# Optimization experiments

Hardware: AMD Instinct MI355X
Metric: run time of the kernel (lower is better)

The kernel has to match this reference:

```python
import jax, jax.numpy as jnp
from jax import lax
import numpy as np

B, C, H, W = 32, 256, 56, 56
R = max(1, C // 16)  # reduced channels = 16
K = 7                # spatial kernel


def setup_inputs() -> dict:
    key = jax.random.key(0)
    k_x, k1, k2, k3 = jax.random.split(key, 4)
    x = jax.random.normal(k_x, (B, C, H, W), dtype=jnp.float32)
    # shared MLP 1x1 convs (bias=False): stored as 2D matrices
    w1 = jax.random.normal(k1, (R, C), dtype=jnp.float32) * (1.0 / np.sqrt(C))
    w2 = jax.random.normal(k2, (C, R), dtype=jnp.float32) * (1.0 / np.sqrt(R))
    # spatial 7x7 conv: 2 in-channels (avg,max) -> 1 out, OIHW
    w_sp = jax.random.normal(k3, (1, 2, K, K), dtype=jnp.float32) * (1.0 / np.sqrt(2 * K * K))
    return {"x": x, "w1": w1, "w2": w2, "w_sp": w_sp}


def reference(x, w1, w2, w_sp):
    # ---- Channel attention ----
    avg = jnp.mean(x, axis=(2, 3))            # (B, C)
    mx = jnp.max(x, axis=(2, 3))              # (B, C)

    def mlp(v):  # shared 1x1-conv MLP on pooled vectors
        return jnp.einsum('cr,br->bc', w2, jax.nn.relu(jnp.einsum('rc,bc->br', w1, v)))

    ca = jax.nn.sigmoid(mlp(avg) + mlp(mx))[:, :, None, None]  # (B, C, 1, 1)
    xc = x * ca                                # (B, C, H, W)

    # ---- Spatial attention ----
    pooled = jnp.stack([jnp.mean(xc, axis=1), jnp.max(xc, axis=1)], axis=1)  # (B, 2, H, W)
    pad = (K - 1) // 2
    sa = jax.nn.sigmoid(
        lax.conv_general_dilated(pooled, w_sp, window_strides=(1, 1),
                                 padding=[(pad, pad), (pad, pad)],
                                 dimension_numbers=('NCHW', 'OIHW', 'NCHW')))  # (B, 1, H, W)

    # ---- Residual ----
    return x + xc * sa
```

## Files before the change

kernel.cpp:

```cpp
#include <hip/hip_runtime.h>
#include <math.h>

#define B_ 32
#define C_ 256
#define H_ 56
#define W_ 56
#define HW_ (H_*W_)
#define R_ 16
#define K_ 7

__device__ __forceinline__ float sigmoidf_(float v) { return 1.0f / (1.0f + expf(-v)); }

__global__ void k_pool_bc(const float* __restrict__ x,
                          float* __restrict__ avg, float* __restrict__ mx) {
    const int bc = blockIdx.x;
    const float4* xp = (const float4*)(x + (size_t)bc * HW_);
    float s = 0.0f, m = -INFINITY;
    for (int i = threadIdx.x; i < HW_ / 4; i += blockDim.x) {
        float4 v = xp[i];
        s += v.x + v.y + v.z + v.w;
        m = fmaxf(m, fmaxf(fmaxf(v.x, v.y), fmaxf(v.z, v.w)));
    }
    #pragma unroll
    for (int off = 32; off > 0; off >>= 1) {
        s += __shfl_down(s, off, 64);
        m  = fmaxf(m, __shfl_down(m, off, 64));
    }
    __shared__ float ss[4], sm[4];
    const int wave = threadIdx.x >> 6;
    if ((threadIdx.x & 63) == 0) { ss[wave] = s; sm[wave] = m; }
    __syncthreads();
    if (threadIdx.x == 0) {
        float S = ss[0] + ss[1] + ss[2] + ss[3];
        float M = fmaxf(fmaxf(sm[0], sm[1]), fmaxf(sm[2], sm[3]));
        avg[bc] = S * (1.0f / HW_);
        mx[bc]  = M;
    }
}

__global__ void k_mlp_ca(const float* __restrict__ avg, const float* __restrict__ mx,
                         const float* __restrict__ w1, const float* __restrict__ w2,
                         float* __restrict__ ca) {
    const int b = blockIdx.x;
    __shared__ float sa_[C_], sm_[C_], h_[R_];
    const int t = threadIdx.x;
    sa_[t] = avg[b * C_ + t];
    sm_[t] = mx[b * C_ + t];
    __syncthreads();
    if (t < R_) {
        float ha = 0.0f, hm = 0.0f;
        for (int c = 0; c < C_; ++c) {
            const float wv = w1[t * C_ + c];
            ha += wv * sa_[c];
            hm += wv * sm_[c];
        }
        h_[t] = fmaxf(ha, 0.0f) + fmaxf(hm, 0.0f);
    }
    __syncthreads();
    float acc = 0.0f;
    #pragma unroll
    for (int r = 0; r < R_; ++r) acc += w2[t * R_ + r] * h_[r];
    ca[b * C_ + t] = sigmoidf_(acc);
}

__global__ void k_spatial_pool(const float* __restrict__ x, const float* __restrict__ ca,
                               float* __restrict__ pooled) {
    const int idx = blockIdx.x * blockDim.x + threadIdx.x;
    if (idx >= B_ * (HW_ / 4)) return;
    const int b = idx / (HW_ / 4);
    const int q = idx % (HW_ / 4);
    const float4* xp = (const float4*)(x + (size_t)b * C_ * HW_);
    const float* cab = ca + b * C_;
    float4 s = {0.f, 0.f, 0.f, 0.f};
    float4 m = {-INFINITY, -INFINITY, -INFINITY, -INFINITY};
    for (int c = 0; c < C_; ++c) {
        const float a = cab[c];
        float4 v = xp[c * (HW_ / 4) + q];
        v.x *= a; v.y *= a; v.z *= a; v.w *= a;
        s.x += v.x; s.y += v.y; s.z += v.z; s.w += v.w;
        m.x = fmaxf(m.x, v.x); m.y = fmaxf(m.y, v.y);
        m.z = fmaxf(m.z, v.z); m.w = fmaxf(m.w, v.w);
    }
    const float inv = 1.0f / C_;
    float4 sm4 = {s.x * inv, s.y * inv, s.z * inv, s.w * inv};
    ((float4*)(pooled + (size_t)b * 2 * HW_))[q]      = sm4;
    ((float4*)(pooled + (size_t)b * 2 * HW_ + HW_))[q] = m;
}

__global__ void k_conv_sa(const float* __restrict__ pooled, const float* __restrict__ wsp,
                          float* __restrict__ sa) {
    __shared__ float wv[2 * K_ * K_];
    if (threadIdx.x < 2 * K_ * K_) wv[threadIdx.x] = wsp[threadIdx.x];
    __syncthreads();
    const int idx = blockIdx.x * blockDim.x + threadIdx.x;
    if (idx >= B_ * HW_) return;
    const int b = idx / HW_;
    const int hw = idx % HW_;
    const int h = hw / W_, w = hw % W_;
    const float* pa = pooled + (size_t)b * 2 * HW_;
    const float* pm = pa + HW_;
    float acc = 0.0f;
    #pragma unroll
    for (int ky = 0; ky < K_; ++ky) {
        const int y = h + ky - 3;
        if (y < 0 || y >= H_) continue;
        #pragma unroll
        for (int kx = 0; kx < K_; ++kx) {
            const int xx = w + kx - 3;
            if (xx < 0 || xx >= W_) continue;
            const int o = y * W_ + xx;
            acc += wv[ky * K_ + kx] * pa[o] + wv[K_ * K_ + ky * K_ + kx] * pm[o];
        }
    }
    sa[idx] = sigmoidf_(acc);
}

__global__ void k_finalize(const float* __restrict__ x, const float* __restrict__ ca,
                           const float* __restrict__ sa, float* __restrict__ out) {
    const size_t idx = (size_t)blockIdx.x * blockDim.x + threadIdx.x;
    if (idx >= (size_t)B_ * C_ * (HW_ / 4)) return;
    const size_t e = idx * 4;
    const int b  = (int)(e / ((size_t)C_ * HW_));
    const int c  = (int)((e / HW_) % C_);
    const int hw = (int)(e % HW_);
    const float a = ca[b * C_ + c];
    const float4 s4 = *(const float4*)(sa + (size_t)b * HW_ + hw);
    const float4 v  = *(const float4*)(x + e);
    float4 o;
    o.x = v.x * (1.0f + a * s4.x);
    o.y = v.y * (1.0f + a * s4.y);
    o.z = v.z * (1.0f + a * s4.z);
    o.w = v.w * (1.0f + a * s4.w);
    *(float4*)((float*)out + e) = o;
}

extern "C" void kernel_launch(void* const* d_in, const int* in_sizes, int n_in,
                              void* d_out, int out_size, void* d_ws, size_t ws_size,
                              hipStream_t stream) {
    const float* x   = (const float*)d_in[0];
    const float* w1  = (const float*)d_in[1];
    const float* w2  = (const float*)d_in[2];
    const float* wsp = (const float*)d_in[3];
    float* out = (float*)d_out;

    float* ws    = (float*)d_ws;
    float* avg    = ws;
    float* mx     = avg + B_ * C_;
    float* ca     = mx + B_ * C_;
    float* pooled = ca + B_ * C_;
    float* sa     = pooled + (size_t)B_ * 2 * HW_;

    k_pool_bc<<<B_ * C_, 256, 0, stream>>>(x, avg, mx);
    k_mlp_ca<<<B_, C_, 0, stream>>>(avg, mx, w1, w2, ca);
    {
        const int n = B_ * (HW_ / 4);
        k_spatial_pool<<<(n + 255) / 256, 256, 0, stream>>>(x, ca, pooled);
    }
    {
        const int n = B_ * HW_;
        k_conv_sa<<<(n + 255) / 256, 256, 0, stream>>>(pooled, wsp, sa);
    }
    {
        const size_t n = (size_t)B_ * C_ * (HW_ / 4);
        k_finalize<<<(int)((n + 255) / 256), 256, 0, stream>>>(x, ca, sa, out);
    }
}
```

Baseline: 244.5 us.

## Split spatial channel pooling across 16 channel groups with shared-memory tree reduce

The spatial pooling kernel previously gave each thread a full 256-channel serial loop and launched only about 200 blocks. Now each block covers 16 float4 positions of one batch, with 16 thread groups each reducing 16 channels before a shared-memory tree combines the partial sums and maxima. This raises parallelism and memory-level concurrency for the large read of x. In exchange it adds shared-memory traffic and barriers, and each warp now reads only 256-byte contiguous segments per channel.

```diff
diff --git a/kernel.cpp b/kernel.cpp
--- a/kernel.cpp
+++ b/kernel.cpp
@@ -6,6 +6,7 @@
 #define H_ 56
 #define W_ 56
 #define HW_ (H_*W_)
+#define Q_ (HW_/4)
 #define R_ 16
 #define K_ 7
 
@@ -16,7 +17,7 @@
     const int bc = blockIdx.x;
     const float4* xp = (const float4*)(x + (size_t)bc * HW_);
     float s = 0.0f, m = -INFINITY;
-    for (int i = threadIdx.x; i < HW_ / 4; i += blockDim.x) {
+    for (int i = threadIdx.x; i < Q_; i += blockDim.x) {
         float4 v = xp[i];
         s += v.x + v.y + v.z + v.w;
         m = fmaxf(m, fmaxf(fmaxf(v.x, v.y), fmaxf(v.z, v.w)));
@@ -63,28 +64,54 @@
     ca[b * C_ + t] = sigmoidf_(acc);
 }
 
-__global__ void k_spatial_pool(const float* __restrict__ x, const float* __restrict__ ca,
-                               float* __restrict__ pooled) {
-    const int idx = blockIdx.x * blockDim.x + threadIdx.x;
-    if (idx >= B_ * (HW_ / 4)) return;
-    const int b = idx / (HW_ / 4);
-    const int q = idx % (HW_ / 4);
+__global__ void __launch_bounds__(256)
+k_spatial_pool(const float* __restrict__ x, const float* __restrict__ ca,
+               float* __restrict__ pooled) {
+    const int b  = blockIdx.y;
+    const int q0 = blockIdx.x * 16;
+    const int t  = threadIdx.x;
+    const int tq = t & 15;
+    const int tc = t >> 4;
+    const int q  = q0 + tq;
+
     const float4* xp = (const float4*)(x + (size_t)b * C_ * HW_);
     const float* cab = ca + b * C_;
+
     float4 s = {0.f, 0.f, 0.f, 0.f};
     float4 m = {-INFINITY, -INFINITY, -INFINITY, -INFINITY};
-    for (int c = 0; c < C_; ++c) {
+    #pragma unroll 4
+    for (int i = 0; i < 16; ++i) {
+        const int c = tc * 16 + i;
         const float a = cab[c];
-        float4 v = xp[c * (HW_ / 4) + q];
+        float4 v = xp[(size_t)c * Q_ + q];
         v.x *= a; v.y *= a; v.z *= a; v.w *= a;
         s.x += v.x; s.y += v.y; s.z += v.z; s.w += v.w;
         m.x = fmaxf(m.x, v.x); m.y = fmaxf(m.y, v.y);
         m.z = fmaxf(m.z, v.z); m.w = fmaxf(m.w, v.w);
     }
-    const float inv = 1.0f / C_;
-    float4 sm4 = {s.x * inv, s.y * inv, s.z * inv, s.w * inv};
-    ((float4*)(pooled + (size_t)b * 2 * HW_))[q]      = sm4;
-    ((float4*)(pooled + (size_t)b * 2 * HW_ + HW_))[q] = m;
+
+    __shared__ float4 ls[256];
+    __shared__ float4 lm[256];
+    ls[t] = s; lm[t] = m;
+    __syncthreads();
+    #pragma unroll
+    for (int st = 8; st >= 1; st >>= 1) {
+        if (tc < st) {
+            const int o = t + st * 16;
+            float4 os = ls[o], om = lm[o];
+            s.x += os.x; s.y += os.y; s.z += os.z; s.w += os.w;
+            m.x = fmaxf(m.x, om.x); m.y = fmaxf(m.y, om.y);
+            m.z = fmaxf(m.z, om.z); m.w = fmaxf(m.w, om.w);
+            ls[t] = s; lm[t] = m;
+        }
+        __syncthreads();
+    }
+    if (tc == 0) {
+        const float inv = 1.0f / C_;
+        float4 sm4 = {s.x * inv, s.y * inv, s.z * inv, s.w * inv};
+        ((float4*)(pooled + (size_t)b * 2 * HW_))[q]       = sm4;
+        ((float4*)(pooled + (size_t)b * 2 * HW_ + HW_))[q] = m;
+    }
 }
 
 __global__ void k_conv_sa(const float* __restrict__ pooled, const float* __restrict__ wsp,
@@ -118,7 +145,7 @@
 __global__ void k_finalize(const float* __restrict__ x, const float* __restrict__ ca,
                            const float* __restrict__ sa, float* __restrict__ out) {
     const size_t idx = (size_t)blockIdx.x * blockDim.x + threadIdx.x;
-    if (idx >= (size_t)B_ * C_ * (HW_ / 4)) return;
+    if (idx >= (size_t)B_ * C_ * Q_) return;
     const size_t e = idx * 4;
     const int b  = (int)(e / ((size_t)C_ * HW_));
     const int c  = (int)((e / HW_) % C_);
@@ -143,7 +170,7 @@
     const float* wsp = (const float*)d_in[3];
     float* out = (float*)d_out;
 
-    float* ws    = (float*)d_ws;
+    float* ws     = (float*)d_ws;
     float* avg    = ws;
     float* mx     = avg + B_ * C_;
     float* ca     = mx + B_ * C_;
@@ -153,15 +180,15 @@
     k_pool_bc<<<B_ * C_, 256, 0, stream>>>(x, avg, mx);
     k_mlp_ca<<<B_, C_, 0, stream>>>(avg, mx, w1, w2, ca);
     {
-        const int n = B_ * (HW_ / 4);
-        k_spatial_pool<<<(n + 255) / 256, 256, 0, stream>>>(x, ca, pooled);
+        dim3 g(Q_ / 16, B_);
+        k_spatial_pool<<<g, 256, 0, stream>>>(x, ca, pooled);
     }
     {
         const int n = B_ * HW_;
         k_conv_sa<<<(n + 255) / 256, 256, 0, stream>>>(pooled, wsp, sa);
     }
     {
-        const size_t n = (size_t)B_ * C_ * (HW_ / 4);
+        const size_t n = (size_t)B_ * C_ * Q_;
         k_finalize<<<(int)((n + 255) / 256), 256, 0, stream>>>(x, ca, sa, out);
     }
 }
```

After: 233.3 us. 4.6% less time.
